# Kernel tuning notes

Hardware: AMD Instinct MI355X
Metric: run time of the kernel (lower is better)

Reference implementation:

```python
import jax, jax.numpy as jnp
import numpy as np

B, C, H, W = 64, 64, 32, 32
K = 1024  # codebook_num
EPS = 1e-10


def setup_inputs() -> dict:
    key = jax.random.key(0)
    kz, kc = jax.random.split(key)
    z = jax.random.normal(kz, (B, C, H, W), dtype=jnp.float32)
    # nn.init.uniform_(codebook.weight, -1/K, 1/K)
    codebook = jax.random.uniform(kc, (K, C), dtype=jnp.float32, minval=-1.0 / K, maxval=1.0 / K)
    return {"z": z, "codebook": codebook}


def reference(z, codebook):
    Bz, Cz, Hz, Wz = z.shape
    flat_z = jnp.transpose(z, (0, 2, 3, 1)).reshape(-1, Cz)  # [N, C]
    dists = (jnp.sum(flat_z ** 2, axis=1, keepdims=True)
             + jnp.sum(codebook ** 2, axis=1)
             - 2.0 * flat_z @ codebook.T)
    indices = jnp.argmin(dists, axis=1)  # [N] int
    quantized_z = codebook[indices].reshape(Bz, Hz, Wz, Cz).transpose(0, 3, 1, 2)
    quantized_z_st = z + jax.lax.stop_gradient(quantized_z - z)
    # perplexity: probs = mean one-hot = histogram / N
    n = indices.shape[0]
    counts = jax.ops.segment_sum(jnp.ones((n,), dtype=jnp.float32), indices, num_segments=K)
    probs = counts / n
    perplexity = jnp.exp(-jnp.sum(probs * jnp.log(jnp.clip(probs, EPS))))
    return quantized_z, quantized_z_st, indices, perplexity
```

## Files before the change

kernel.cpp:

```cpp
#include <hip/hip_runtime.h>
#include <math.h>

#define NVEC   65536
#define CDIM   64
#define KBOOK  1024
#define NTOT   4194304


typedef _Float16 f16x8 __attribute__((ext_vector_type(8)));
typedef float    f32x4 __attribute__((ext_vector_type(4)));

#define FORP(M) M(0) M(1) M(2) M(3)

__global__ void prep_kernel(const float* __restrict__ cb, float* __restrict__ se,
                            int* __restrict__ hist, _Float16* __restrict__ cbT,
                            float* __restrict__ se16, float* __restrict__ semax4,
                            unsigned* __restrict__ wcount, float* __restrict__ cbt) {
    __shared__ float lmax[4];
    const int t = blockIdx.x * 256 + threadIdx.x;
    if (t == 0) *wcount = 0u;
    hist[t] = 0;
    const float* row = cb + t * CDIM;
    float r[8];
#pragma unroll
    for (int j = 0; j < 8; ++j) r[j] = __fmul_rn(row[j], row[j]);
#pragma unroll
    for (int i = 8; i < 64; i += 8)
#pragma unroll
        for (int j = 0; j < 8; ++j) r[j] = __fadd_rn(r[j], __fmul_rn(row[i + j], row[i + j]));
    const float sev = __fadd_rn(__fadd_rn(__fadd_rn(r[0], r[1]), __fadd_rn(r[2], r[3])),
                                __fadd_rn(__fadd_rn(r[4], r[5]), __fadd_rn(r[6], r[7])));
    se[t] = sev;
    se16[t] = sev * 16384.0f;
    float m = sev;
#pragma unroll
    for (int off = 32; off > 0; off >>= 1) m = fmaxf(m, __shfl_xor(m, off));
    if ((threadIdx.x & 63) == 0) lmax[threadIdx.x >> 6] = m;
    __syncthreads();
    if (threadIdx.x == 0)
        semax4[blockIdx.x] = fmaxf(fmaxf(lmax[0], lmax[1]), fmaxf(lmax[2], lmax[3]));
#pragma unroll
    for (int c = 0; c < 64; ++c) cbt[c * 1024 + t] = row[c];
    const int tt = t >> 4, la = t & 15;
    _Float16* tb = cbT + (size_t)tt * 1024;
#pragma unroll
    for (int g = 0; g < 4; ++g)
#pragma unroll
        for (int j = 0; j < 8; ++j) {
            const float e0 = row[8 * g + j] * 16384.0f;
            const float e1 = row[32 + 8 * g + j] * 16384.0f;
            const int lo8 = (g * 16 + la) * 8 + j;
            tb[lo8]       = (_Float16)e0;
            tb[512 + lo8] = (_Float16)e1;
        }
}

__launch_bounds__(256)
__attribute__((amdgpu_waves_per_eu(4, 4)))
__global__ void approx_kernel(const float* __restrict__ z, const _Float16* __restrict__ cbT,
                              const float* __restrict__ se16, const float* __restrict__ semax4,
                              unsigned* __restrict__ result, unsigned* __restrict__ wlist,
                              unsigned* __restrict__ wcount, float* __restrict__ outIdxF,
                              int* __restrict__ hist) {
    __shared__ unsigned m1[4][4][16], m2[4][4][16];
    const int tid = threadIdx.x;
    const int w = tid >> 6;
    const int l = tid & 63;
    const int la = l & 15;
    const int g  = l >> 4;
    const int nbase = blockIdx.x * 64;

#define ZPRE(p)                                                          \
    f16x8 mh0_##p, mh1_##p; float psum_##p = 0.0f; {                     \
        const int n_ = nbase + (p) * 16 + la;                            \
        const int b_ = n_ >> 10, hw_ = n_ & 1023;                        \
        const float* zb_ = z + (size_t)b_ * (CDIM * 1024) + hw_;         \
        _Pragma("unroll")                                                \
        for (int j = 0; j < 8; ++j) {                                    \
            { float zc = zb_[(g * 8 + j) * 1024];                        \
              mh0_##p[j] = (_Float16)(-2.0f * zc);                       \
              psum_##p = fmaf(zc, zc, psum_##p); }                       \
            { float zc = zb_[(32 + g * 8 + j) * 1024];                   \
              mh1_##p[j] = (_Float16)(-2.0f * zc);                       \
              psum_##p = fmaf(zc, zc, psum_##p); }                       \
        } }
    FORP(ZPRE)
#undef ZPRE

#define KINIT(p) unsigned u1k_##p = 0xFFFFFFFFu, u2k_##p = 0xFFFFFFFFu;
    FORP(KINIT)
#undef KINIT

    const int kv = g * 4;
    const _Float16* tbase = cbT + (size_t)l * 8;

#define DECL_SLOT(s) f16x8 ah0_##s, ah1_##s; f32x4 se_##s;
    DECL_SLOT(a) DECL_SLOT(b)
#undef DECL_SLOT

#define LOADT(s, ttv) { const int t_ = (ttv) & 63;                       \
        const _Float16* p_ = tbase + (size_t)t_ * 1024;                  \
        ah0_##s = *(const f16x8*)(p_);                                   \
        ah1_##s = *(const f16x8*)(p_ + 512);                             \
        se_##s  = *(const f32x4*)(se16 + t_ * 16 + kv); }

#define COMP1(s, p, k0_) {                                               \
        f32x4 acc = se_##s;                                              \
        acc = __builtin_amdgcn_mfma_f32_16x16x32_f16(ah0_##s, mh0_##p, acc, 0, 0, 0); \
        acc = __builtin_amdgcn_mfma_f32_16x16x32_f16(ah1_##s, mh1_##p, acc, 0, 0, 0); \
        _Pragma("unroll")                                                \
        for (int r_ = 0; r_ < 4; ++r_) {                                 \
            unsigned ub = __float_as_uint(acc[r_]);                      \
            ub = ((int)ub < 0) ? ~ub : (ub | 0x80000000u);               \
            const unsigned key = (ub & 0xFFFFFC00u) | (unsigned)((k0_) + r_); \
            const unsigned mx = (u1k_##p > key) ? u1k_##p : key;         \
            u1k_##p = (u1k_##p < key) ? u1k_##p : key;                   \
            u2k_##p = (u2k_##p < mx) ? u2k_##p : mx;                     \
        } }

#define COMPT(s, ttv) { const int k0_ = (ttv) * 16 + kv;                 \
        COMP1(s, 0, k0_) COMP1(s, 1, k0_) COMP1(s, 2, k0_) COMP1(s, 3, k0_) }

    const int t0 = w * 16;
    LOADT(a, t0)
    for (int tt = t0; tt < t0 + 16; tt += 2) {
        LOADT(b, tt + 1)
        COMPT(a, tt)
        LOADT(a, tt + 2)
        COMPT(b, tt + 1)
    }
#undef LOADT
#undef COMP1
#undef COMPT

#define BFLY(p) {                                                        \
        _Pragma("unroll")                                                \
        for (int off = 16; off <= 32; off <<= 1) {                       \
            const unsigned p1 = __shfl_xor(u1k_##p, off);                \
            const unsigned p2 = __shfl_xor(u2k_##p, off);                \
            psum_##p += __shfl_xor(psum_##p, off);                       \
            const unsigned mx = (u1k_##p > p1) ? u1k_##p : p1;           \
            u1k_##p = (u1k_##p < p1) ? u1k_##p : p1;                     \
            const unsigned mm = (u2k_##p < p2) ? u2k_##p : p2;           \
            u2k_##p = (mm < mx) ? mm : mx;                               \
        } }
    FORP(BFLY)
#undef BFLY

    if (l < 16) {
#define STOREM(p) m1[w][p][l] = u1k_##p; m2[w][p][l] = u2k_##p;
        FORP(STOREM)
#undef STOREM
    }
    __syncthreads();

    if (tid < 64) {
        const int p = tid >> 4, la2 = tid & 15;
        float sx = psum_0;
        if (p == 1) sx = psum_1;
        else if (p == 2) sx = psum_2;
        else if (p == 3) sx = psum_3;
        unsigned u1 = m1[0][p][la2], u2 = m2[0][p][la2];
#pragma unroll
        for (int ww = 1; ww < 4; ++ww) {
            const unsigned o1 = m1[ww][p][la2], o2 = m2[ww][p][la2];
            const unsigned mx = (u1 > o1) ? u1 : o1;
            u1 = (u1 < o1) ? u1 : o1;
            unsigned t2 = (u2 < o2) ? u2 : o2;
            u2 = (t2 < mx) ? t2 : mx;
        }

        const float srt = sqrtf(fmaxf(fmaxf(semax4[0], semax4[1]),
                                      fmaxf(semax4[2], semax4[3]))) * 1.0001f;
        const float THR = 60.2f * sqrtf(sx) * srt + 1.97e-2f * sx + 0.165f;
        const unsigned x1 = u1 & 0xFFFFFC00u, x2 = u2 & 0xFFFFFC00u;
        const float f1 = __uint_as_float((x1 & 0x80000000u) ? (x1 & 0x7FFFFFFFu) : ~x1);
        const float f2 = __uint_as_float((x2 & 0x80000000u) ? (x2 & 0x7FFFFFFFu) : ~x2);
        const int k1 = (int)(u1 & 1023u);
        const int n = nbase + tid;
        if (f2 - f1 > THR) {
            result[n] = (unsigned)k1;
            outIdxF[n] = (float)k1;
            atomicAdd(&hist[k1], 1);
        } else {
            const unsigned widx = atomicAdd(wcount, 1u);
            wlist[widx] = (unsigned)n;
        }
    }
}

__launch_bounds__(256)
__global__ void rescore2_kernel(const float* __restrict__ z, const float* __restrict__ cbt,
                                const float* __restrict__ se,
                                const unsigned* __restrict__ wlist,
                                const unsigned* __restrict__ wcount,
                                unsigned* __restrict__ result, int* __restrict__ hist,
                                float* __restrict__ outIdxF) {
    __shared__ float zxs[4][64];
    __shared__ float rres[4][8];
    __shared__ float sxs[4];
    __shared__ unsigned long long red[4][4];
    const int cnt = (int)*wcount;
    const int tid = threadIdx.x;
    const int wv = tid >> 6, l = tid & 63;

    for (int base = blockIdx.x * 4; base < cnt; base += gridDim.x * 4) {
        const int ns = tid >> 6, c = tid & 63;
        const int item = base + ns;
        const int n = (int)wlist[(item < cnt) ? item : base];
        {
            const int b = n >> 10, hw = n & 1023;
            const float zc = z[(size_t)b * (CDIM * 1024) + c * 1024 + hw];
            zxs[ns][c] = zc + zc;
        }
        __syncthreads();
        if (c < 8) {
            const float z0 = zxs[ns][c] * 0.5f;
            float rr = __fmul_rn(z0, z0);
            for (int i = c + 8; i < 64; i += 8) {
                const float zi = zxs[ns][i] * 0.5f;
                rr = __fadd_rn(rr, __fmul_rn(zi, zi));
            }
            rres[ns][c] = rr;
        }
        __syncthreads();
        if (c == 0) {
            const float* r = rres[ns];
            sxs[ns] = __fadd_rn(__fadd_rn(__fadd_rn(r[0], r[1]), __fadd_rn(r[2], r[3])),
                                __fadd_rn(__fadd_rn(r[4], r[5]), __fadd_rn(r[6], r[7])));
        }
        __syncthreads();

        unsigned long long best0 = ~0ull, best1 = ~0ull, best2 = ~0ull, best3 = ~0ull;
        for (int chunk = 0; chunk < 4; ++chunk) {
            const int k = (chunk << 8) + tid;
            float a0 = 0.f, a1 = 0.f, a2 = 0.f, a3 = 0.f;
#pragma unroll 2
            for (int c4 = 0; c4 < 16; ++c4) {
                const float e0 = cbt[(4 * c4 + 0) * 1024 + k];
                const float e1 = cbt[(4 * c4 + 1) * 1024 + k];
                const float e2 = cbt[(4 * c4 + 2) * 1024 + k];
                const float e3 = cbt[(4 * c4 + 3) * 1024 + k];
                const f32x4 z0 = *(const f32x4*)&zxs[0][4 * c4];
                const f32x4 z1 = *(const f32x4*)&zxs[1][4 * c4];
                const f32x4 z2 = *(const f32x4*)&zxs[2][4 * c4];
                const f32x4 z3 = *(const f32x4*)&zxs[3][4 * c4];
                a0 = fmaf(z0[0], e0, a0); a0 = fmaf(z0[1], e1, a0);
                a0 = fmaf(z0[2], e2, a0); a0 = fmaf(z0[3], e3, a0);
                a1 = fmaf(z1[0], e0, a1); a1 = fmaf(z1[1], e1, a1);
                a1 = fmaf(z1[2], e2, a1); a1 = fmaf(z1[3], e3, a1);
                a2 = fmaf(z2[0], e0, a2); a2 = fmaf(z2[1], e1, a2);
                a2 = fmaf(z2[2], e2, a2); a2 = fmaf(z2[3], e3, a2);
                a3 = fmaf(z3[0], e0, a3); a3 = fmaf(z3[1], e1, a3);
                a3 = fmaf(z3[2], e2, a3); a3 = fmaf(z3[3], e3, a3);
            }
            const float sek = se[k];
#define DKEY(ai, bi) { const float d_ = __fsub_rn(__fadd_rn(sxs[bi], sek), ai);    \
        unsigned ob = __float_as_uint(d_);                                         \
        ob = (ob & 0x80000000u) ? ~ob : (ob | 0x80000000u);                        \
        const unsigned long long key = ((unsigned long long)ob << 32) | (unsigned)k; \
        if (key < best##bi) best##bi = key; }
            DKEY(a0, 0) DKEY(a1, 1) DKEY(a2, 2) DKEY(a3, 3)
#undef DKEY
        }

#define WRED(bi) {                                                       \
        unsigned long long b_ = best##bi;                                \
        _Pragma("unroll")                                                \
        for (int off = 1; off <= 32; off <<= 1) {                        \
            const unsigned long long o = __shfl_xor(b_, off);            \
            if (o < b_) b_ = o;                                          \
        }                                                                \
        if (l == 0) red[wv][bi] = b_; }
        WRED(0) WRED(1) WRED(2) WRED(3)
#undef WRED
        __syncthreads();
        if (tid < 4 && base + tid < cnt) {
            unsigned long long bb = red[0][tid];
            if (red[1][tid] < bb) bb = red[1][tid];
            if (red[2][tid] < bb) bb = red[2][tid];
            if (red[3][tid] < bb) bb = red[3][tid];
            const int n2 = (int)wlist[base + tid];
            const int kb = (int)(bb & 0xFFFFFFFFull);
            result[n2] = (unsigned)kb;
            outIdxF[n2] = (float)kb;
            atomicAdd(&hist[kb], 1);
        }
        __syncthreads();
    }
}

__global__ void scatter_kernel(const float* __restrict__ z, const float* __restrict__ cb,
                               const unsigned* __restrict__ result,
                               const int* __restrict__ hist,
                               float* __restrict__ out) {
    const int o = (blockIdx.x * 256 + threadIdx.x) * 4;
    const int b = o >> 16, c = (o >> 10) & 63, hw = o & 1023;
    const int n = (b << 10) | hw;
    float q[4];
#pragma unroll
    for (int j = 0; j < 4; ++j) {
        const int k = (int)result[n + j];
        q[j] = cb[k * CDIM + c];
    }
    const float4 zv = *(const float4*)(z + o);
    *(float4*)(out + o) = make_float4(q[0], q[1], q[2], q[3]);
    float4 st;
    st.x = __fadd_rn(zv.x, __fsub_rn(q[0], zv.x));
    st.y = __fadd_rn(zv.y, __fsub_rn(q[1], zv.y));
    st.z = __fadd_rn(zv.z, __fsub_rn(q[2], zv.z));
    st.w = __fadd_rn(zv.w, __fsub_rn(q[3], zv.w));
    *(float4*)(out + NTOT + o) = st;

    if (blockIdx.x == 0) {
        __shared__ double partial[4];
        const int t = threadIdx.x;
        double term = 0.0;
#pragma unroll
        for (int j = 0; j < 4; ++j) {
            const int cnt = hist[t + 256 * j];
            if (cnt > 0) { const double p = (double)cnt / (double)NVEC; term += p * log(p); }
        }
        for (int off = 32; off > 0; off >>= 1) term += __shfl_down(term, off);
        if ((t & 63) == 0) partial[t >> 6] = term;
        __syncthreads();
        if (t == 0) {
            const double sm = partial[0] + partial[1] + partial[2] + partial[3];
            out[2 * NTOT + NVEC] = (float)exp(-sm);
        }
    }
}

extern "C" void kernel_launch(void* const* d_in, const int* in_sizes, int n_in,
                              void* d_out, int out_size, void* d_ws, size_t ws_size,
                              hipStream_t stream) {
    const float* z  = (const float*)d_in[0];
    const float* cb = (const float*)d_in[1];
    float* out = (float*)d_out;

    char* ws = (char*)d_ws;
    unsigned* result = (unsigned*)ws;
    float* se   = (float*)(ws + 524288);
    int*   hist = (int*)(ws + 528384);

    char* outB = (char*)d_out;
    _Float16* cbT   = (_Float16*)(outB + (1 << 20));
    unsigned* wcount = (unsigned*)(outB + 1572864);
    float*    semax4 = (float*)(outB + 1572864 + 16);
    float*    se16   = (float*)(outB + 1572864 + 4096);
    unsigned* wlist  = (unsigned*)(outB + (2 << 20));
    float*    cbt    = (float*)(outB + (2 << 20) + (512 << 10));

    float* outIdxF = out + 2 * NTOT;

    prep_kernel<<<4, 256, 0, stream>>>(cb, se, hist, cbT, se16, semax4, wcount, cbt);
    approx_kernel<<<NVEC / 64, 256, 0, stream>>>(z, cbT, se16, semax4, result, wlist,
                                                 wcount, outIdxF, hist);
    rescore2_kernel<<<1024, 256, 0, stream>>>(z, cbt, se, wlist, wcount, result,
                                              hist, outIdxF);
    scatter_kernel<<<NTOT / 1024, 256, 0, stream>>>(z, cb, result, hist, out);
}
```

Measured before the change: 166.8 us.

## Split codebook scan over eight waves and bias distances positive for cheaper keys

The approximate nearest-code kernel now runs 512 threads per block, each of eight waves scanning 128 codes instead of 256, and the LDS reduction is widened to match. A +4096 bias added to the scaled codebook norms keeps the MFMA distances positive, so the float-to-sortable-uint flip can be dropped and keys come straight from the raw bits. The manual double-buffered loads are replaced by a simple loop. The acceptance threshold is loosened and a guard on sx sends large-norm vectors to exact rescoring, which may enlarge the fallback list and risks fp16 precision loss from the bias.

```diff
diff --git a/kernel.cpp b/kernel.cpp
--- a/kernel.cpp
+++ b/kernel.cpp
@@ -31,7 +31,7 @@
     const float sev = __fadd_rn(__fadd_rn(__fadd_rn(r[0], r[1]), __fadd_rn(r[2], r[3])),
                                 __fadd_rn(__fadd_rn(r[4], r[5]), __fadd_rn(r[6], r[7])));
     se[t] = sev;
-    se16[t] = sev * 16384.0f;
+    se16[t] = sev * 16384.0f + 4096.0f;
     float m = sev;
 #pragma unroll
     for (int off = 32; off > 0; off >>= 1) m = fmaxf(m, __shfl_xor(m, off));
@@ -55,14 +55,14 @@
         }
 }
 
-__launch_bounds__(256)
-__attribute__((amdgpu_waves_per_eu(4, 4)))
+__launch_bounds__(512)
+__attribute__((amdgpu_waves_per_eu(8)))
 __global__ void approx_kernel(const float* __restrict__ z, const _Float16* __restrict__ cbT,
                               const float* __restrict__ se16, const float* __restrict__ semax4,
                               unsigned* __restrict__ result, unsigned* __restrict__ wlist,
                               unsigned* __restrict__ wcount, float* __restrict__ outIdxF,
                               int* __restrict__ hist) {
-    __shared__ unsigned m1[4][4][16], m2[4][4][16];
+    __shared__ unsigned m1[8][4][16], m2[8][4][16];
     const int tid = threadIdx.x;
     const int w = tid >> 6;
     const int l = tid & 63;
@@ -94,44 +94,29 @@
     const int kv = g * 4;
     const _Float16* tbase = cbT + (size_t)l * 8;
 
-#define DECL_SLOT(s) f16x8 ah0_##s, ah1_##s; f32x4 se_##s;
-    DECL_SLOT(a) DECL_SLOT(b)
-#undef DECL_SLOT
-
-#define LOADT(s, ttv) { const int t_ = (ttv) & 63;                       \
-        const _Float16* p_ = tbase + (size_t)t_ * 1024;                  \
-        ah0_##s = *(const f16x8*)(p_);                                   \
-        ah1_##s = *(const f16x8*)(p_ + 512);                             \
-        se_##s  = *(const f32x4*)(se16 + t_ * 16 + kv); }
-
-#define COMP1(s, p, k0_) {                                               \
-        f32x4 acc = se_##s;                                              \
-        acc = __builtin_amdgcn_mfma_f32_16x16x32_f16(ah0_##s, mh0_##p, acc, 0, 0, 0); \
-        acc = __builtin_amdgcn_mfma_f32_16x16x32_f16(ah1_##s, mh1_##p, acc, 0, 0, 0); \
+#define COMP1(p, k0_) {                                                  \
+        f32x4 acc = sev_;                                                \
+        acc = __builtin_amdgcn_mfma_f32_16x16x32_f16(ah0, mh0_##p, acc, 0, 0, 0); \
+        acc = __builtin_amdgcn_mfma_f32_16x16x32_f16(ah1, mh1_##p, acc, 0, 0, 0); \
         _Pragma("unroll")                                                \
         for (int r_ = 0; r_ < 4; ++r_) {                                 \
-            unsigned ub = __float_as_uint(acc[r_]);                      \
-            ub = ((int)ub < 0) ? ~ub : (ub | 0x80000000u);               \
-            const unsigned key = (ub & 0xFFFFFC00u) | (unsigned)((k0_) + r_); \
+            const unsigned key = (__float_as_uint(acc[r_]) & 0xFFFFFC00u) \
+                                 | (unsigned)((k0_) + r_);               \
             const unsigned mx = (u1k_##p > key) ? u1k_##p : key;         \
             u1k_##p = (u1k_##p < key) ? u1k_##p : key;                   \
             u2k_##p = (u2k_##p < mx) ? u2k_##p : mx;                     \
         } }
 
-#define COMPT(s, ttv) { const int k0_ = (ttv) * 16 + kv;                 \
-        COMP1(s, 0, k0_) COMP1(s, 1, k0_) COMP1(s, 2, k0_) COMP1(s, 3, k0_) }
-
-    const int t0 = w * 16;
-    LOADT(a, t0)
-    for (int tt = t0; tt < t0 + 16; tt += 2) {
-        LOADT(b, tt + 1)
-        COMPT(a, tt)
-        LOADT(a, tt + 2)
-        COMPT(b, tt + 1)
-    }
-#undef LOADT
+    const int t0 = w * 8;
+    for (int tt = t0; tt < t0 + 8; ++tt) {
+        const _Float16* p_ = tbase + (size_t)tt * 1024;
+        const f16x8 ah0 = *(const f16x8*)(p_);
+        const f16x8 ah1 = *(const f16x8*)(p_ + 512);
+        const f32x4 sev_ = *(const f32x4*)(se16 + tt * 16 + kv);
+        const int k0b = tt * 16 + kv;
+        COMP1(0, k0b) COMP1(1, k0b) COMP1(2, k0b) COMP1(3, k0b)
+    }
 #undef COMP1
-#undef COMPT
 
 #define BFLY(p) {                                                        \
         _Pragma("unroll")                                                \
@@ -162,7 +147,7 @@
         else if (p == 3) sx = psum_3;
         unsigned u1 = m1[0][p][la2], u2 = m2[0][p][la2];
 #pragma unroll
-        for (int ww = 1; ww < 4; ++ww) {
+        for (int ww = 1; ww < 8; ++ww) {
             const unsigned o1 = m1[ww][p][la2], o2 = m2[ww][p][la2];
             const unsigned mx = (u1 > o1) ? u1 : o1;
             u1 = (u1 < o1) ? u1 : o1;
@@ -172,13 +157,12 @@
 
         const float srt = sqrtf(fmaxf(fmaxf(semax4[0], semax4[1]),
                                       fmaxf(semax4[2], semax4[3]))) * 1.0001f;
-        const float THR = 60.2f * sqrtf(sx) * srt + 1.97e-2f * sx + 0.165f;
-        const unsigned x1 = u1 & 0xFFFFFC00u, x2 = u2 & 0xFFFFFC00u;
-        const float f1 = __uint_as_float((x1 & 0x80000000u) ? (x1 & 0x7FFFFFFFu) : ~x1);
-        const float f2 = __uint_as_float((x2 & 0x80000000u) ? (x2 & 0x7FFFFFFFu) : ~x2);
+        const float THR = 60.2f * sqrtf(sx) * srt + 1.97e-2f * sx + 1.25f;
+        const float f1 = __uint_as_float(u1 & 0xFFFFFC00u);
+        const float f2 = __uint_as_float(u2 & 0xFFFFFC00u);
         const int k1 = (int)(u1 & 1023u);
         const int n = nbase + tid;
-        if (f2 - f1 > THR) {
+        if (f2 - f1 > THR && sx <= 200.0f) {
             result[n] = (unsigned)k1;
             outIdxF[n] = (float)k1;
             atomicAdd(&hist[k1], 1);
@@ -354,7 +338,7 @@
     float* outIdxF = out + 2 * NTOT;
 
     prep_kernel<<<4, 256, 0, stream>>>(cb, se, hist, cbT, se16, semax4, wcount, cbt);
-    approx_kernel<<<NVEC / 64, 256, 0, stream>>>(z, cbT, se16, semax4, result, wlist,
+    approx_kernel<<<NVEC / 64, 512, 0, stream>>>(z, cbT, se16, semax4, result, wlist,
                                                  wcount, outIdxF, hist);
     rescore2_kernel<<<1024, 256, 0, stream>>>(z, cbt, se, wlist, wcount, result,
                                               hist, outIdxF);
```

After: 242.6 us. 1.45x slower.
